# Performance work log

Hardware: AMD Instinct MI355X
Metric: run time of the kernel (lower is better)

Reference implementation:

```python
import jax, jax.numpy as jnp
import numpy as np

B, N, F_IN, F_OUT = 8, 2048, 128, 128


def setup_inputs() -> dict:
    key = jax.random.key(0)
    k1, k2, k3, k4 = jax.random.split(key, 4)
    h = jax.random.normal(k1, (B, N, F_IN), dtype=jnp.float32)
    adj = (jax.random.uniform(k2, (B, N, N)) > 0.5).astype(jnp.float32)
    adj = jnp.maximum(adj, jnp.eye(N, dtype=jnp.float32)[None])
    # torch nn.Linear weights: W is [out_features, in_features], a is [1, 2*out_features]
    W = jax.random.normal(k3, (F_OUT, F_IN), dtype=jnp.float32) * 0.05
    a = jax.random.normal(k4, (1, 2 * F_OUT), dtype=jnp.float32) * 0.05
    return {"h": h, "adj": adj, "W": W, "a": a}


def reference(h, adj, W, a):
    # Wh = W(h): [B, N, F_OUT]
    Wh = jnp.einsum("bnf,of->bno", h, W)
    # attn_fc(concat(Wh_i, Wh_j)) == (Wh_i @ a1) + (Wh_j @ a2): exact split of the
    # linear layer, avoiding the O(B*N*N*2F) concat intermediate.
    a1 = a[0, :F_OUT]
    a2 = a[0, F_OUT:]
    e_i = Wh @ a1  # [B, N]  score contribution of destination node i
    e_j = Wh @ a2  # [B, N]  score contribution of source node j
    e = e_i[:, :, None] + e_j[:, None, :]  # [B, N, N]
    e = e + (1.0 - adj) * (-1e9)
    alpha = jax.nn.softmax(e, axis=-1)  # [B, N, N]
    # weighted aggregation: h_out[b,i] = sum_j alpha[b,i,j] * Wh[b,j]
    h_out = jnp.einsum("bij,bjo->bio", alpha, Wh)
    return h_out
```

## Files before the change

kernel.cpp:

```cpp
#include <hip/hip_runtime.h>
#include <stdint.h>

#define AS1 __attribute__((address_space(1)))
#define AS3 __attribute__((address_space(3)))

typedef __bf16 bf16x8 __attribute__((ext_vector_type(8)));
typedef float f32x4 __attribute__((ext_vector_type(4)));

constexpr int NB = 8;
constexpr int N  = 2048;
constexpr int F  = 128;

__device__ __forceinline__ unsigned short bf16r(float f) {
    unsigned u = __float_as_uint(f);
    return (unsigned short)((u + 0x7FFFu + ((u >> 16) & 1u)) >> 16);
}
__device__ __forceinline__ float bf2f(unsigned short s) {
    return __uint_as_float(((unsigned)s) << 16);
}


__global__ __launch_bounds__(256) void k1_wh(const float* __restrict__ h,
                                             const float* __restrict__ W,
                                             const float* __restrict__ a,
                                             unsigned short* __restrict__ Wb2,
                                             unsigned short* __restrict__ p16) {
    __shared__ float epart[2][64];

    const int tid  = threadIdx.x;
    const int lane = tid & 63, wid = tid >> 6;
    const int quad = lane >> 4, l15 = lane & 15;
    const int wm = wid >> 1, wn = wid & 1;
    const int m0 = blockIdx.x * 64;
    const int batch = m0 >> 11;
    const int nbase = m0 & 2047;

    f32x4 acc[2][4] = {};

#pragma unroll
    for (int kk = 0; kk < 4; ++kk) {
        const int k = kk * 32 + quad * 8;
        bf16x8 afr[2], bfr[4];
#pragma unroll
        for (int rt = 0; rt < 2; ++rt) {
            const float* src = h + (size_t)(m0 + wm * 32 + rt * 16 + l15) * F + k;
            float4 x0 = *(const float4*)src;
            float4 x1 = *(const float4*)(src + 4);
            afr[rt][0] = (__bf16)x0.x; afr[rt][1] = (__bf16)x0.y;
            afr[rt][2] = (__bf16)x0.z; afr[rt][3] = (__bf16)x0.w;
            afr[rt][4] = (__bf16)x1.x; afr[rt][5] = (__bf16)x1.y;
            afr[rt][6] = (__bf16)x1.z; afr[rt][7] = (__bf16)x1.w;
        }
#pragma unroll
        for (int ct = 0; ct < 4; ++ct) {
            const int o = wn * 64 + ct * 16 + l15;
            const float* src = W + (size_t)o * F + k;
            float4 x0 = *(const float4*)src;
            float4 x1 = *(const float4*)(src + 4);
            bfr[ct][0] = (__bf16)x0.x; bfr[ct][1] = (__bf16)x0.y;
            bfr[ct][2] = (__bf16)x0.z; bfr[ct][3] = (__bf16)x0.w;
            bfr[ct][4] = (__bf16)x1.x; bfr[ct][5] = (__bf16)x1.y;
            bfr[ct][6] = (__bf16)x1.z; bfr[ct][7] = (__bf16)x1.w;
        }
#pragma unroll
        for (int rt = 0; rt < 2; ++rt)
#pragma unroll
            for (int ct = 0; ct < 4; ++ct)
                acc[rt][ct] = __builtin_amdgcn_mfma_f32_16x16x32_bf16(
                    afr[rt], bfr[ct], acc[rt][ct], 0, 0, 0);
    }

    float a2v[4];
#pragma unroll
    for (int ct = 0; ct < 4; ++ct) a2v[ct] = a[F + wn * 64 + ct * 16 + l15];

    float ep[2][4];
#pragma unroll
    for (int rt = 0; rt < 2; ++rt)
#pragma unroll
        for (int g = 0; g < 4; ++g) {
            float s = 0.f;
#pragma unroll
            for (int ct = 0; ct < 4; ++ct) s += acc[rt][ct][g] * a2v[ct];
            ep[rt][g] = s;
        }
#pragma unroll
    for (int m = 1; m < 16; m <<= 1)
#pragma unroll
        for (int rt = 0; rt < 2; ++rt)
#pragma unroll
            for (int g = 0; g < 4; ++g)
                ep[rt][g] += __shfl_xor(ep[rt][g], m);

    if (l15 == 0)
#pragma unroll
        for (int rt = 0; rt < 2; ++rt)
#pragma unroll
            for (int g = 0; g < 4; ++g)
                epart[wn][wm * 32 + rt * 16 + quad * 4 + g] = ep[rt][g];
    __syncthreads();

#pragma unroll
    for (int rt = 0; rt < 2; ++rt)
#pragma unroll
        for (int ct = 0; ct < 4; ++ct) {
            const int o  = wn * 64 + ct * 16 + l15;
            const int r0 = wm * 32 + rt * 16 + quad * 4;
            const int n0 = nbase + r0;
            ushort4 v;
#pragma unroll
            for (int g = 0; g < 4; ++g) {
                const float e  = epart[0][r0 + g] + epart[1][r0 + g];
                const float pf = bf2f(bf16r(expf(e)));
                (&v.x)[g] = bf16r(pf * acc[rt][ct][g]);
            }
            size_t off = (size_t)batch * N * F + (size_t)(n0 >> 3) * 1024 + o * 8 + (n0 & 7);
            *(ushort4*)&Wb2[off] = v;
        }

    if (tid < 64) {
        const float e = epart[0][tid] + epart[1][tid];
        p16[batch * N + nbase + tid] = bf16r(expf(e));
    }
}

__global__ __launch_bounds__(512, 2) void k3_fused(const float* __restrict__ adj,
                                                   const unsigned short* __restrict__ Wb2,
                                                   const unsigned short* __restrict__ p16,
                                                   float* __restrict__ out) {
    __shared__ __align__(16) char Asm_[3][16384];
    __shared__ __align__(16) char Bsm_[3][16384];
    __shared__ __align__(16) char Psm_[4096];

    const int tid  = threadIdx.x;
    const int lane = tid & 63, wid = tid >> 6;
    const int quad = lane >> 4, l15 = lane & 15;
    const int wr = wid >> 2, wc = wid & 3;
    const int b  = blockIdx.x & 7;
    const int it = blockIdx.x >> 3;
    const int i0 = it * 64;

    const float* aSrc[2];
#pragma unroll
    for (int s = 0; s < 2; ++s) {
        const int rl = (wid * 2 + s) * 4 + (lane >> 4);
        const int G  = (lane & 15) ^ (rl & 15);
        aSrc[s] = adj + (size_t)b * N * N + (size_t)(i0 + rl) * N + G * 4;
    }
    const char* bSrc = (const char*)Wb2 + (size_t)b * (N * F * 2)
                     + wid * 2048 + lane * 16;
    const char* pSrc = (const char*)p16 + (size_t)b * N * 2 + lane * 16;

#define K3_STAGE(BI, C)                                                            \
    do {                                                                           \
        __builtin_amdgcn_global_load_lds((const AS1 void*)(aSrc[0] + (C) * 64),    \
            (AS3 void*)(&Asm_[BI][(wid * 2 + 0) * 1024]), 16, 0, 0);               \
        __builtin_amdgcn_global_load_lds((const AS1 void*)(aSrc[1] + (C) * 64),    \
            (AS3 void*)(&Asm_[BI][(wid * 2 + 1) * 1024]), 16, 0, 0);               \
        __builtin_amdgcn_global_load_lds(                                          \
            (const AS1 void*)(bSrc + (size_t)(C) * 16384 + 0 * 1024),              \
            (AS3 void*)(&Bsm_[BI][wid * 2048 + 0 * 1024]), 16, 0, 0);              \
        __builtin_amdgcn_global_load_lds(                                          \
            (const AS1 void*)(bSrc + (size_t)(C) * 16384 + 1 * 1024),              \
            (AS3 void*)(&Bsm_[BI][wid * 2048 + 1 * 1024]), 16, 0, 0);              \
    } while (0)

    f32x4 acc[2][2] = {};
    f32x4 dacc[2] = {};

    if (wid == 0) {
#pragma unroll
        for (int s = 0; s < 4; ++s)
            __builtin_amdgcn_global_load_lds((const AS1 void*)(pSrc + s * 1024),
                (AS3 void*)(&Psm_[s * 1024]), 16, 0, 0);
    }
    K3_STAGE(0, 0);
    K3_STAGE(1, 1);
    K3_STAGE(2, 2);

#define K3_CHUNK(C, BI, WAITSTR, DOSTAGE)                                          \
    {                                                                              \
        asm volatile(WAITSTR ::: "memory");                                        \
        __builtin_amdgcn_s_barrier();                                              \
        __builtin_amdgcn_sched_barrier(0);                                         \
        const char* aB = &Asm_[BI][0];                                             \
        const char* bB = &Bsm_[BI][0];                                             \
        _Pragma("unroll")                                                          \
        for (int ks = 0; ks < 2; ++ks) {                                           \
            bf16x8 pv = *(const bf16x8*)(&Psm_[(C) * 128 + ks * 64 + quad * 16]);  \
            bf16x8 af[2];                                                          \
            _Pragma("unroll")                                                      \
            for (int rt = 0; rt < 2; ++rt) {                                       \
                const int row = wr * 32 + rt * 16 + l15;                           \
                const int G0  = ks * 8 + quad * 2;                                 \
                f32x4 x0 = *(const f32x4*)(aB + row * 256                          \
                              + (((G0 + 0) ^ (row & 15)) << 4));                   \
                f32x4 x1 = *(const f32x4*)(aB + row * 256                          \
                              + (((G0 + 1) ^ (row & 15)) << 4));                   \
                af[rt][0] = (__bf16)x0[0]; af[rt][1] = (__bf16)x0[1];              \
                af[rt][2] = (__bf16)x0[2]; af[rt][3] = (__bf16)x0[3];              \
                af[rt][4] = (__bf16)x1[0]; af[rt][5] = (__bf16)x1[1];              \
                af[rt][6] = (__bf16)x1[2]; af[rt][7] = (__bf16)x1[3];              \
            }                                                                      \
            _Pragma("unroll")                                                      \
            for (int ct = 0; ct < 2; ++ct) {                                       \
                bf16x8 bf = *(const bf16x8*)(bB + (ks * 4 + quad) * 2048           \
                                + (wc * 32 + ct * 16) * 16 + l15 * 16);            \
                acc[0][ct] = __builtin_amdgcn_mfma_f32_16x16x32_bf16(              \
                    af[0], bf, acc[0][ct], 0, 0, 0);                               \
                acc[1][ct] = __builtin_amdgcn_mfma_f32_16x16x32_bf16(              \
                    af[1], bf, acc[1][ct], 0, 0, 0);                               \
            }                                                                      \
            dacc[0] = __builtin_amdgcn_mfma_f32_16x16x32_bf16(                     \
                af[0], pv, dacc[0], 0, 0, 0);                                      \
            dacc[1] = __builtin_amdgcn_mfma_f32_16x16x32_bf16(                     \
                af[1], pv, dacc[1], 0, 0, 0);                                      \
        }                                                                          \
        if (DOSTAGE) {                                                             \
            __builtin_amdgcn_s_barrier();                                          \
            __builtin_amdgcn_sched_barrier(0);                                     \
            K3_STAGE(BI, (C) + 3);                                                 \
        }                                                                          \
    }

    for (int c3 = 0; c3 < 27; c3 += 3) {
        K3_CHUNK(c3 + 0, 0, "s_waitcnt vmcnt(8)", 1)
        K3_CHUNK(c3 + 1, 1, "s_waitcnt vmcnt(8)", 1)
        K3_CHUNK(c3 + 2, 2, "s_waitcnt vmcnt(8)", 1)
    }
    K3_CHUNK(27, 0, "s_waitcnt vmcnt(8)", 1)
    K3_CHUNK(28, 1, "s_waitcnt vmcnt(8)", 1)
    K3_CHUNK(29, 2, "s_waitcnt vmcnt(8)", 0)
    K3_CHUNK(30, 0, "s_waitcnt vmcnt(4)", 0)
    K3_CHUNK(31, 1, "s_waitcnt vmcnt(0)", 0)

#undef K3_CHUNK
#undef K3_STAGE

#pragma unroll
    for (int rt = 0; rt < 2; ++rt)
#pragma unroll
        for (int g = 0; g < 4; ++g) {
            const float inv = 1.0f / dacc[rt][g];
            float* orow = out + ((size_t)b * N + i0 + wr * 32 + rt * 16
                                 + quad * 4 + g) * F + wc * 32 + l15;
            orow[0]  = acc[rt][0][g] * inv;
            orow[16] = acc[rt][1][g] * inv;
        }
}

extern "C" void kernel_launch(void* const* d_in, const int* in_sizes, int n_in,
                              void* d_out, int out_size, void* d_ws, size_t ws_size,
                              hipStream_t stream) {
    const float* h   = (const float*)d_in[0];
    const float* adj = (const float*)d_in[1];
    const float* W   = (const float*)d_in[2];
    const float* a   = (const float*)d_in[3];
    float* out = (float*)d_out;

    unsigned short* Wb2 = (unsigned short*)d_ws;
    unsigned short* p16 = (unsigned short*)((char*)d_ws + (4u << 20));

    k1_wh<<<NB * N / 64, 256, 0, stream>>>(h, W, a, Wb2, p16);
    k3_fused<<<NB * 32, 512, 0, stream>>>(adj, Wb2, p16, out);
}
```

Baseline: 217.5 us.

## Pack adjacency into bitmask in first kernel and expand bits to bf16 in MFMA kernel

Extra blocks added to the first kernel threshold the fp32 adjacency and pack it into a bitmask (one bit per entry) with wave ballots. The fused attention kernel then stages the whole 64-row bitmask in LDS once and builds the bf16 0/1 A-fragments from bits, instead of streaming fp32 adjacency tiles through LDS every chunk. The full adj matrix is still read once, but the large k3 kernel loses its dominant global stream and the fp32-to-bf16 conversion work. In exchange there is an extra write and read of the mask and some bit-manipulation ALU work per fragment.

```diff
diff --git a/kernel.cpp b/kernel.cpp
--- a/kernel.cpp
+++ b/kernel.cpp
@@ -6,6 +6,7 @@
 
 typedef __bf16 bf16x8 __attribute__((ext_vector_type(8)));
 typedef float f32x4 __attribute__((ext_vector_type(4)));
+typedef unsigned int u32x4 __attribute__((ext_vector_type(4)));
 
 constexpr int NB = 8;
 constexpr int N  = 2048;
@@ -20,15 +21,40 @@
 }
 
 
-__global__ __launch_bounds__(256) void k1_wh(const float* __restrict__ h,
-                                             const float* __restrict__ W,
-                                             const float* __restrict__ a,
-                                             unsigned short* __restrict__ Wb2,
-                                             unsigned short* __restrict__ p16) {
-    __shared__ float epart[2][64];
-
+__global__ __launch_bounds__(256) void k01_wh(const float* __restrict__ h,
+                                              const float* __restrict__ adj,
+                                              const float* __restrict__ W,
+                                              const float* __restrict__ a,
+                                              unsigned short* __restrict__ Wb2,
+                                              unsigned short* __restrict__ p16,
+                                              unsigned char* __restrict__ maskG) {
     const int tid  = threadIdx.x;
     const int lane = tid & 63, wid = tid >> 6;
+
+    if (blockIdx.x >= 256) {
+        const int cid = blockIdx.x - 256;
+#pragma unroll
+        for (int rr = 0; rr < 2; ++rr) {
+            const int row = cid * 8 + wid * 2 + rr;
+            const float2* src = (const float2*)(adj + (size_t)row * 2048) + lane;
+            u32x4* dst = (u32x4*)(maskG + (size_t)row * 256);
+#pragma unroll 4
+            for (int t = 0; t < 16; ++t) {
+                float2 v = src[t * 64];
+                unsigned long long m0 = __ballot(v.x > 0.5f);
+                unsigned long long m1 = __ballot(v.y > 0.5f);
+                if (lane == 0) {
+                    u32x4 w = { (unsigned)m0, (unsigned)(m0 >> 32),
+                                (unsigned)m1, (unsigned)(m1 >> 32) };
+                    dst[t] = w;
+                }
+            }
+        }
+        return;
+    }
+
+    __shared__ float epart[2][64];
+
     const int quad = lane >> 4, l15 = lane & 15;
     const int wm = wid >> 1, wn = wid & 1;
     const int m0 = blockIdx.x * 64;
@@ -124,13 +150,13 @@
     }
 }
 
-__global__ __launch_bounds__(512, 2) void k3_fused(const float* __restrict__ adj,
+__global__ __launch_bounds__(512, 2) void k3_fused(const unsigned char* __restrict__ maskG,
                                                    const unsigned short* __restrict__ Wb2,
                                                    const unsigned short* __restrict__ p16,
                                                    float* __restrict__ out) {
-    __shared__ __align__(16) char Asm_[3][16384];
     __shared__ __align__(16) char Bsm_[3][16384];
     __shared__ __align__(16) char Psm_[4096];
+    __shared__ __align__(16) char Msm_[16384];
 
     const int tid  = threadIdx.x;
     const int lane = tid & 63, wid = tid >> 6;
@@ -140,23 +166,28 @@
     const int it = blockIdx.x >> 3;
     const int i0 = it * 64;
 
-    const float* aSrc[2];
-#pragma unroll
-    for (int s = 0; s < 2; ++s) {
-        const int rl = (wid * 2 + s) * 4 + (lane >> 4);
-        const int G  = (lane & 15) ^ (rl & 15);
-        aSrc[s] = adj + (size_t)b * N * N + (size_t)(i0 + rl) * N + G * 4;
-    }
+    const int mr = tid >> 3;
+    const int tp = (tid & 7) * 2;
+    const u32x4* mg = (const u32x4*)(maskG + ((size_t)(b * 2048 + i0 + mr)) * 256
+                                     + (size_t)tp * 16);
+    u32x4 mv0 = mg[0];
+    u32x4 mv1 = mg[1];
+    if (wid == 0) {
+        const char* pSrc = (const char*)p16 + (size_t)b * N * 2 + lane * 16;
+#pragma unroll
+        for (int s = 0; s < 4; ++s)
+            __builtin_amdgcn_global_load_lds((const AS1 void*)(pSrc + s * 1024),
+                (AS3 void*)(&Psm_[s * 1024]), 16, 0, 0);
+    }
+    *(u32x4*)&Msm_[mr * 256 + (((tp + 0) + mr) & 15) * 16] = mv0;
+    *(u32x4*)&Msm_[mr * 256 + (((tp + 1) + mr) & 15) * 16] = mv1;
+    __syncthreads();
+
     const char* bSrc = (const char*)Wb2 + (size_t)b * (N * F * 2)
                      + wid * 2048 + lane * 16;
-    const char* pSrc = (const char*)p16 + (size_t)b * N * 2 + lane * 16;
 
 #define K3_STAGE(BI, C)                                                            \
     do {                                                                           \
-        __builtin_amdgcn_global_load_lds((const AS1 void*)(aSrc[0] + (C) * 64),    \
-            (AS3 void*)(&Asm_[BI][(wid * 2 + 0) * 1024]), 16, 0, 0);               \
-        __builtin_amdgcn_global_load_lds((const AS1 void*)(aSrc[1] + (C) * 64),    \
-            (AS3 void*)(&Asm_[BI][(wid * 2 + 1) * 1024]), 16, 0, 0);               \
         __builtin_amdgcn_global_load_lds(                                          \
             (const AS1 void*)(bSrc + (size_t)(C) * 16384 + 0 * 1024),              \
             (AS3 void*)(&Bsm_[BI][wid * 2048 + 0 * 1024]), 16, 0, 0);              \
@@ -168,12 +199,6 @@
     f32x4 acc[2][2] = {};
     f32x4 dacc[2] = {};
 
-    if (wid == 0) {
-#pragma unroll
-        for (int s = 0; s < 4; ++s)
-            __builtin_amdgcn_global_load_lds((const AS1 void*)(pSrc + s * 1024),
-                (AS3 void*)(&Psm_[s * 1024]), 16, 0, 0);
-    }
     K3_STAGE(0, 0);
     K3_STAGE(1, 1);
     K3_STAGE(2, 2);
@@ -183,24 +208,32 @@
         asm volatile(WAITSTR ::: "memory");                                        \
         __builtin_amdgcn_s_barrier();                                              \
         __builtin_amdgcn_sched_barrier(0);                                         \
-        const char* aB = &Asm_[BI][0];                                             \
         const char* bB = &Bsm_[BI][0];                                             \
+          \
+        unsigned uE[2], uO[2];                                                     \
+        _Pragma("unroll")                                                          \
+        for (int rt = 0; rt < 2; ++rt) {                                           \
+            const int row = wr * 32 + rt * 16 + l15;                               \
+            u32x4 q = *(const u32x4*)&Msm_[row * 256                               \
+                          + (((((C) >> 1)) + row) & 15) * 16];                     \
+            uE[rt] = ((C) & 1) ? q.y : q.x;                                        \
+            uO[rt] = ((C) & 1) ? q.w : q.z;                                        \
+        }                                                                          \
         _Pragma("unroll")                                                          \
         for (int ks = 0; ks < 2; ++ks) {                                           \
             bf16x8 pv = *(const bf16x8*)(&Psm_[(C) * 128 + ks * 64 + quad * 16]);  \
             bf16x8 af[2];                                                          \
             _Pragma("unroll")                                                      \
             for (int rt = 0; rt < 2; ++rt) {                                       \
-                const int row = wr * 32 + rt * 16 + l15;                           \
-                const int G0  = ks * 8 + quad * 2;                                 \
-                f32x4 x0 = *(const f32x4*)(aB + row * 256                          \
-                              + (((G0 + 0) ^ (row & 15)) << 4));                   \
-                f32x4 x1 = *(const f32x4*)(aB + row * 256                          \
-                              + (((G0 + 1) ^ (row & 15)) << 4));                   \
-                af[rt][0] = (__bf16)x0[0]; af[rt][1] = (__bf16)x0[1];              \
-                af[rt][2] = (__bf16)x0[2]; af[rt][3] = (__bf16)x0[3];              \
-                af[rt][4] = (__bf16)x1[0]; af[rt][5] = (__bf16)x1[1];              \
-                af[rt][6] = (__bf16)x1[2]; af[rt][7] = (__bf16)x1[3];              \
+                const int base = ks * 16 + quad * 4;                               \
+                u32x4 aw;                                                          \
+                _Pragma("unroll")                                                  \
+                for (int i = 0; i < 4; ++i) {                                      \
+                    const int bi = base + i;                                       \
+                    aw[i] = (((uE[rt] >> bi) & 1u) ? 0x00003F80u : 0u)             \
+                          | (((uO[rt] >> bi) & 1u) ? 0x3F800000u : 0u);            \
+                }                                                                  \
+                af[rt] = __builtin_bit_cast(bf16x8, aw);                           \
             }                                                                      \
             _Pragma("unroll")                                                      \
             for (int ct = 0; ct < 2; ++ct) {                                       \
@@ -224,14 +257,14 @@
     }
 
     for (int c3 = 0; c3 < 27; c3 += 3) {
-        K3_CHUNK(c3 + 0, 0, "s_waitcnt vmcnt(8)", 1)
-        K3_CHUNK(c3 + 1, 1, "s_waitcnt vmcnt(8)", 1)
-        K3_CHUNK(c3 + 2, 2, "s_waitcnt vmcnt(8)", 1)
-    }
-    K3_CHUNK(27, 0, "s_waitcnt vmcnt(8)", 1)
-    K3_CHUNK(28, 1, "s_waitcnt vmcnt(8)", 1)
-    K3_CHUNK(29, 2, "s_waitcnt vmcnt(8)", 0)
-    K3_CHUNK(30, 0, "s_waitcnt vmcnt(4)", 0)
+        K3_CHUNK(c3 + 0, 0, "s_waitcnt vmcnt(4)", 1)
+        K3_CHUNK(c3 + 1, 1, "s_waitcnt vmcnt(4)", 1)
+        K3_CHUNK(c3 + 2, 2, "s_waitcnt vmcnt(4)", 1)
+    }
+    K3_CHUNK(27, 0, "s_waitcnt vmcnt(4)", 1)
+    K3_CHUNK(28, 1, "s_waitcnt vmcnt(4)", 1)
+    K3_CHUNK(29, 2, "s_waitcnt vmcnt(4)", 0)
+    K3_CHUNK(30, 0, "s_waitcnt vmcnt(2)", 0)
     K3_CHUNK(31, 1, "s_waitcnt vmcnt(0)", 0)
 
 #undef K3_CHUNK
@@ -258,9 +291,10 @@
     const float* a   = (const float*)d_in[3];
     float* out = (float*)d_out;
 
-    unsigned short* Wb2 = (unsigned short*)d_ws;
-    unsigned short* p16 = (unsigned short*)((char*)d_ws + (4u << 20));
-
-    k1_wh<<<NB * N / 64, 256, 0, stream>>>(h, W, a, Wb2, p16);
-    k3_fused<<<NB * 32, 512, 0, stream>>>(adj, Wb2, p16, out);
-}
+    unsigned short* Wb2  = (unsigned short*)d_ws;
+    unsigned short* p16  = (unsigned short*)((char*)d_ws + (4u << 20));
+    unsigned char*  maskG = (unsigned char*)((char*)d_ws + (8u << 20));
+
+    k01_wh<<<256 + 2048, 256, 0, stream>>>(h, adj, W, a, Wb2, p16, maskG);
+    k3_fused<<<NB * 32, 512, 0, stream>>>(maskG, Wb2, p16, out);
+}
```

Result: slower. 242.4 us (+11.4%).
